# Kernel optimization log

Hardware: AMD Instinct MI355X
Metric: run time of the kernel (lower is better)

Reference implementation:

```python
import jax, jax.numpy as jnp
import numpy as np

B, H, S, D = 4, 16, 2048, 128

def setup_inputs() -> dict:
    key = jax.random.key(0)
    k1, k2, k3, k4 = jax.random.split(key, 4)
    query = jax.random.normal(k1, (B, H, S, D), dtype=jnp.float32)
    key_t = jax.random.normal(k2, (B, H, S, D), dtype=jnp.float32)
    value = jax.random.normal(k3, (B, H, S, D), dtype=jnp.float32)
    mask = jax.random.randint(k4, (B, 1, S, S), 0, 2, dtype=jnp.int32)
    return {"query": query, "key": key_t, "value": value, "mask": mask}

def reference(query, key, value, mask):
    d_k = query.shape[-1]
    scale = d_k ** 0.5
    # [B,H,S,S] attention logits
    attn_logits = jnp.einsum('bhqd,bhkd->bhqk', query, key)
    neg_inf = jnp.finfo(attn_logits.dtype).min
    attn_logits = jnp.where(mask == 0, neg_inf, attn_logits)
    attn_weights = jax.nn.softmax(attn_logits / scale, axis=-1)
    # dropout is identity in eval/inference mode
    attn_output = jnp.einsum('bhqk,bhkd->bhqd', attn_weights, value)
    return attn_output, attn_weights
```

## Files before the change

### kernel.cpp

```cpp
#include <hip/hip_runtime.h>
#include <hip/hip_bf16.h>

namespace {

constexpr int Hn = 16;
constexpr int Sn = 2048;
constexpr int Dn = 128;
constexpr int BM = 64;
constexpr int BN = 64;
constexpr int THREADS = 256;
constexpr int NT = Sn / BN;
constexpr long long OUT0 = 4LL * 16 * 2048 * 128;

constexpr int QSTR = 136;
constexpr int VSTR = 68;

typedef short s16x4 __attribute__((ext_vector_type(4)));
typedef float f32x4 __attribute__((ext_vector_type(4)));

__device__ __forceinline__ unsigned short f2bu(float x) {
    return __bfloat16_as_ushort(__float2bfloat16(x));
}
__device__ __forceinline__ unsigned pk2(float lo, float hi) {
    return (unsigned)f2bu(lo) | ((unsigned)f2bu(hi) << 16);
}

__device__ __forceinline__ void k_issue(const float* __restrict__ g, int sc, int sr,
                                        float4* v) {
#pragma unroll
    for (int it = 0; it < 4; ++it) {
        const float4* gp = reinterpret_cast<const float4*>(
            g + (size_t)(sr + 16 * it) * Dn + sc * 8);
        v[2 * it]     = gp[0];
        v[2 * it + 1] = gp[1];
    }
}
__device__ __forceinline__ void k_write(unsigned short* lds, int sc, int sr,
                                        const float4* v) {
#pragma unroll
    for (int it = 0; it < 4; ++it) {
        const int r = sr + 16 * it;
        uint4 u;
        u.x = pk2(v[2 * it].x,     v[2 * it].y);
        u.y = pk2(v[2 * it].z,     v[2 * it].w);
        u.z = pk2(v[2 * it + 1].x, v[2 * it + 1].y);
        u.w = pk2(v[2 * it + 1].z, v[2 * it + 1].w);
        *reinterpret_cast<uint4*>(reinterpret_cast<char*>(lds) + r * (QSTR * 2) + sc * 16) = u;
    }
}

__device__ __forceinline__ void v_issue(const float* __restrict__ g, int tc, int kp,
                                        float4* v) {
#pragma unroll
    for (int it = 0; it < 4; ++it) {
        const int kr = 2 * (kp + 8 * it);
        v[2 * it]     = *reinterpret_cast<const float4*>(g + (size_t)kr * Dn + 4 * tc);
        v[2 * it + 1] = *reinterpret_cast<const float4*>(g + (size_t)(kr + 1) * Dn + 4 * tc);
    }
}
__device__ __forceinline__ void v_write(unsigned short* vt, int tc, int kp,
                                        const float4* v) {
#pragma unroll
    for (int it = 0; it < 4; ++it) {
        const int kr = 2 * (kp + 8 * it);
        const float a4[4] = {v[2 * it].x, v[2 * it].y, v[2 * it].z, v[2 * it].w};
        const float b4[4] = {v[2 * it + 1].x, v[2 * it + 1].y, v[2 * it + 1].z, v[2 * it + 1].w};
#pragma unroll
        for (int j = 0; j < 4; ++j) {
            const int d = 4 * tc + j;
            *reinterpret_cast<unsigned*>(reinterpret_cast<char*>(vt) + d * (VSTR * 2) + kr * 2)
                = pk2(a4[j], b4[j]);
        }
    }
}

struct SAcc { f32x4 t[4]; };

__global__ __launch_bounds__(THREADS)
void attn_fused(const float* __restrict__ Q, const float* __restrict__ K,
                const float* __restrict__ V, const int* __restrict__ M,
                float* __restrict__ out) {
    __shared__ __align__(16) unsigned short smem[8704 * 2 + BM * VSTR];
    unsigned short* bufA = smem;
    unsigned short* bufB = smem + 8704;
    unsigned short* wlds = smem + 17408;

    const int tid  = threadIdx.x;
    const int lane = tid & 63;
    const int wv   = tid >> 6;
    const int lr   = lane & 15;
    const int lg   = lane >> 4;

    const int bh    = blockIdx.y;
    const int b     = bh >> 4;
    const int qbase = blockIdx.x * BM;

    const float* Qg = Q + ((size_t)bh * Sn + qbase) * Dn;
    const float* Kg = K + (size_t)bh * Sn * Dn;
    const float* Vg = V + (size_t)bh * Sn * Dn;
    const int*   Mg = M + ((size_t)b * Sn + qbase) * Sn;
    float*       Og = out + ((size_t)bh * Sn + qbase) * Dn;
    float*       Wg = out + OUT0 + ((size_t)bh * Sn + qbase) * Sn;

    const float scl2 = 1.4426950408889634f / 11.313708498984761f;
    const int qrow = 16 * wv + 4 * lg;

    const int sc = tid & 15, sr = tid >> 4;
    const int tc = tid & 31, kp = tid >> 5;

    const int* mrow[4];
#pragma unroll
    for (int r = 0; r < 4; ++r) mrow[r] = Mg + (size_t)(qrow + r) * Sn + lr;

    {
        float4 qv[8], kv[8];
        k_issue(Qg, sc, sr, qv);
        k_issue(Kg, sc, sr, kv);
        k_write(bufB, sc, sr, qv);
        k_write(bufA, sc, sr, kv);
    }
    __syncthreads();
    s16x4 qf[8];
#pragma unroll
    for (int dsv = 0; dsv < 8; ++dsv)
        qf[dsv] = *reinterpret_cast<const s16x4*>(
            reinterpret_cast<const char*>(bufB) + (16 * wv + lr) * (QSTR * 2) + dsv * 32 + lg * 8);
    __syncthreads();

    const f32x4 zero = {0.f, 0.f, 0.f, 0.f};

    auto qk_tile = [&](const unsigned short* kb) -> SAcc {
        SAcc s;
#pragma unroll
        for (int t = 0; t < 4; ++t) s.t[t] = zero;
#pragma unroll
        for (int dsv = 0; dsv < 8; ++dsv) {
            const int koff = dsv * 32 + lg * 8;
#pragma unroll
            for (int t = 0; t < 4; ++t) {
                const s16x4 bb = *reinterpret_cast<const s16x4*>(
                    reinterpret_cast<const char*>(kb) + (16 * t + lr) * (QSTR * 2) + koff);
                s.t[t] = __builtin_amdgcn_mfma_f32_16x16x16bf16_1k(qf[dsv], bb, s.t[t], 0, 0, 0);
            }
        }
        return s;
    };

    float rs[4] = {0.f, 0.f, 0.f, 0.f};
    for (int t = 0; t < NT; ++t) {
        unsigned short* cur = (t & 1) ? bufB : bufA;
        unsigned short* nxt = (t & 1) ? bufA : bufB;
        float4 kv[8];
        const bool pre = (t + 1 < NT);
        if (pre) k_issue(Kg + (size_t)(t + 1) * BN * Dn, sc, sr, kv);

        int mv[16];
        const int kc = t * BN;
#pragma unroll
        for (int tt = 0; tt < 4; ++tt)
#pragma unroll
            for (int r = 0; r < 4; ++r) mv[4 * tt + r] = mrow[r][kc + 16 * tt];

        SAcc s = qk_tile(cur);
#pragma unroll
        for (int tt = 0; tt < 4; ++tt)
#pragma unroll
            for (int r = 0; r < 4; ++r)
                rs[r] += mv[4 * tt + r] ? __builtin_amdgcn_exp2f(s.t[tt][r] * scl2) : 0.f;

        if (pre) k_write(nxt, sc, sr, kv);
        __syncthreads();
    }

    float inv[4];
#pragma unroll
    for (int r = 0; r < 4; ++r) {
        float v = rs[r];
        v += __shfl_xor(v, 1);
        v += __shfl_xor(v, 2);
        v += __shfl_xor(v, 4);
        v += __shfl_xor(v, 8);
        inv[r] = 1.0f / v;
    }

    {
        float4 kv0[8], vv0[8];
        k_issue(Kg, sc, sr, kv0);
        v_issue(Vg, tc, kp, vv0);
        k_write(bufA, sc, sr, kv0);
        v_write(bufB, tc, kp, vv0);
    }
    __syncthreads();

    f32x4 oacc[8];
#pragma unroll
    for (int f = 0; f < 8; ++f) oacc[f] = zero;

    for (int t = 0; t < NT; ++t) {
        float4 kv[8], vv[8];
        const bool pre = (t + 1 < NT);
        if (pre) {
            k_issue(Kg + (size_t)(t + 1) * BN * Dn, sc, sr, kv);
            v_issue(Vg + (size_t)(t + 1) * BN * Dn, tc, kp, vv);
        }

        int mv[16];
        const int kc = t * BN;
#pragma unroll
        for (int tt = 0; tt < 4; ++tt)
#pragma unroll
            for (int r = 0; r < 4; ++r) mv[4 * tt + r] = mrow[r][kc + 16 * tt];

        SAcc s = qk_tile(bufA);

#pragma unroll
        for (int tt = 0; tt < 4; ++tt) {
#pragma unroll
            for (int r = 0; r < 4; ++r) {
                const float e = mv[4 * tt + r] ? __builtin_amdgcn_exp2f(s.t[tt][r] * scl2) : 0.f;
                const float w = e * inv[r];
                Wg[(size_t)(qrow + r) * Sn + kc + 16 * tt + lr] = w;
                reinterpret_cast<unsigned short*>(
                    reinterpret_cast<char*>(wlds) + (qrow + r) * (VSTR * 2))[16 * tt + lr] = f2bu(w);
            }
        }

#pragma unroll
        for (int kk = 0; kk < 4; ++kk) {
            const int koff = kk * 32 + lg * 8;
            const s16x4 aw = *reinterpret_cast<const s16x4*>(
                reinterpret_cast<const char*>(wlds) + (16 * wv + lr) * (VSTR * 2) + koff);
#pragma unroll
            for (int f = 0; f < 8; ++f) {
                const s16x4 bv = *reinterpret_cast<const s16x4*>(
                    reinterpret_cast<const char*>(bufB) + (16 * f + lr) * (VSTR * 2) + koff);
                oacc[f] = __builtin_amdgcn_mfma_f32_16x16x16bf16_1k(aw, bv, oacc[f], 0, 0, 0);
            }
        }
        __syncthreads();
        if (pre) {
            k_write(bufA, sc, sr, kv);
            v_write(bufB, tc, kp, vv);
        }
        __syncthreads();
    }

#pragma unroll
    for (int f = 0; f < 8; ++f) {
#pragma unroll
        for (int r = 0; r < 4; ++r) {
            Og[(size_t)(qrow + r) * Dn + 16 * f + lr] = oacc[f][r];
        }
    }
}

}

extern "C" void kernel_launch(void* const* d_in, const int* in_sizes, int n_in,
                              void* d_out, int out_size, void* d_ws, size_t ws_size,
                              hipStream_t stream) {
    (void)in_sizes; (void)n_in; (void)d_ws; (void)ws_size; (void)out_size;
    const float* Q = (const float*)d_in[0];
    const float* K = (const float*)d_in[1];
    const float* V = (const float*)d_in[2];
    const int*   M = (const int*)d_in[3];
    float* out = (float*)d_out;
    dim3 grid(Sn / BM, 4 * Hn);
    attn_fused<<<grid, THREADS, 0, stream>>>(Q, K, V, M, out);
}
```

Baseline: 1.006 ms.

## Preconvert Q/K/V to swizzled bf16 and bit-pack mask before attention

Adds pre-pass kernels that convert Q (pre-scaled), K and a transposed V to bf16 in swizzled workspace layouts, and pack the int32 mask into bitmasks. The main attention kernel then streams K/V tiles straight into LDS with global_load_lds DMA double buffering, reads mask bits instead of int32 values, and normalises via a log-sum subtracted in the exponent. This removes the repeated fp32 loads, conversions and mask traffic across the two passes, at the cost of extra launches and workspace traffic. The original kernel is kept as a fallback when the workspace is too small.

```diff
diff --git a/kernel.cpp b/kernel.cpp
--- a/kernel.cpp
+++ b/kernel.cpp
@@ -3,17 +3,21 @@
 
 namespace {
 
-constexpr int Hn = 16;
 constexpr int Sn = 2048;
 constexpr int Dn = 128;
-constexpr int BM = 64;
 constexpr int BN = 64;
 constexpr int THREADS = 256;
 constexpr int NT = Sn / BN;
-constexpr long long OUT0 = 4LL * 16 * 2048 * 128;
-
-constexpr int QSTR = 136;
-constexpr int VSTR = 68;
+constexpr int NH = 64;
+constexpr long long OUT0 = 4LL * 16 * Sn * Dn;
+constexpr float QSs = 1.4426950408889634f / 11.313708498984761f;
+
+constexpr size_t HB     = (size_t)Sn * Dn * 2;
+constexpr size_t QB_OFF = 0;
+constexpr size_t KB_OFF = HB * NH;
+constexpr size_t VT_OFF = 2 * HB * NH;
+constexpr size_t MB_OFF = 3 * HB * NH;
+constexpr size_t WS_NEED = MB_OFF + (size_t)4 * Sn * 64 * 4;
 
 typedef short s16x4 __attribute__((ext_vector_type(4)));
 typedef float f32x4 __attribute__((ext_vector_type(4)));
@@ -25,8 +29,248 @@
     return (unsigned)f2bu(lo) | ((unsigned)f2bu(hi) << 16);
 }
 
-__device__ __forceinline__ void k_issue(const float* __restrict__ g, int sc, int sr,
-                                        float4* v) {
+__device__ __forceinline__ void glds16(const char* g, char* l) {
+    __builtin_amdgcn_global_load_lds(
+        (__attribute__((address_space(1))) void*)(uintptr_t)g,
+        (__attribute__((address_space(3))) void*)(uintptr_t)(unsigned)(uintptr_t)l,
+        16, 0, 0);
+}
+
+#define MFMA16(A, B, C) __builtin_amdgcn_mfma_f32_16x16x16bf16_1k((A), (B), (C), 0, 0, 0)
+
+
+__global__ __launch_bounds__(256) void cvt_rows(const float* __restrict__ src,
+                                                char* __restrict__ dst, float qs) {
+    const int x = blockIdx.x * 256 + threadIdx.x;
+    const int c = x & 15;
+    const int row = x >> 4;
+    const float4* gp = reinterpret_cast<const float4*>(src + (size_t)row * Dn + c * 8);
+    const float4 f0 = gp[0], f1 = gp[1];
+    uint4 u;
+    u.x = pk2(f0.x * qs, f0.y * qs);
+    u.y = pk2(f0.z * qs, f0.w * qs);
+    u.z = pk2(f1.x * qs, f1.y * qs);
+    u.w = pk2(f1.z * qs, f1.w * qs);
+    *reinterpret_cast<uint4*>(dst + (size_t)row * 256 + ((c * 16) ^ ((row & 7) << 4))) = u;
+}
+
+__global__ __launch_bounds__(256) void cvt_vt(const float* __restrict__ V,
+                                              char* __restrict__ vt) {
+    const int x = blockIdx.x * 256 + threadIdx.x;
+    const int d = x & 127;
+    const int kc8 = (x >> 7) & 255;
+    const int bh = x >> 15;
+    const float* s = V + (size_t)bh * Sn * Dn + (size_t)kc8 * 8 * Dn + d;
+    float f[8];
+#pragma unroll
+    for (int i = 0; i < 8; ++i) f[i] = s[(size_t)i * Dn];
+    uint4 u;
+    u.x = pk2(f[0], f[1]); u.y = pk2(f[2], f[3]);
+    u.z = pk2(f[4], f[5]); u.w = pk2(f[6], f[7]);
+    *reinterpret_cast<uint4*>(vt + (size_t)bh * HB + (size_t)(kc8 >> 3) * 16384
+                              + d * 128 + (((kc8 & 7) * 16) ^ ((d & 7) << 4))) = u;
+}
+
+__global__ __launch_bounds__(256) void mask_pack(const int* __restrict__ M,
+                                                 unsigned* __restrict__ mb) {
+    const int x = blockIdx.x * 256 + threadIdx.x;
+    const int w = x & 63;
+    const int q = (x >> 6) & 2047;
+    const int b = x >> 17;
+    const int4* p = reinterpret_cast<const int4*>(M + ((size_t)b * Sn + q) * Sn + w * 32);
+    unsigned u = 0;
+#pragma unroll
+    for (int i = 0; i < 8; ++i) {
+        const int4 v = p[i];
+        u |= (v.x != 0 ? 1u : 0u) << (4 * i);
+        u |= (v.y != 0 ? 1u : 0u) << (4 * i + 1);
+        u |= (v.z != 0 ? 1u : 0u) << (4 * i + 2);
+        u |= (v.w != 0 ? 1u : 0u) << (4 * i + 3);
+    }
+    mb[x] = u;
+}
+
+
+__global__ __launch_bounds__(THREADS, 2)
+void attn_main(const char* __restrict__ ws, const unsigned* __restrict__ mbits,
+               float* __restrict__ out) {
+    __shared__ __align__(16) char smem[74496];
+    char* kb0 = smem;
+    char* kb1 = smem + 16384;
+    char* vb0 = smem + 32768;
+    char* vb1 = smem + 49152;
+    unsigned short* wl = reinterpret_cast<unsigned short*>(smem + 65536);
+
+    const int tid  = threadIdx.x;
+    const int lane = tid & 63;
+    const int wv   = tid >> 6;
+    const int lr   = lane & 15;
+    const int lg   = lane >> 4;
+
+    const int bh    = blockIdx.y;
+    const int b     = bh >> 4;
+    const int qbase = blockIdx.x * 64;
+
+    const char* Qbh  = ws + (size_t)bh * HB;
+    const char* Kbh  = ws + KB_OFF + (size_t)bh * HB;
+    const char* Vtbh = ws + VT_OFF + (size_t)bh * HB;
+    float*      Og   = out + ((size_t)bh * Sn + qbase) * Dn;
+    float*      Wg   = out + OUT0 + ((size_t)bh * Sn + qbase) * Sn;
+
+    const int qrow = 16 * wv + 4 * lg;
+
+    const unsigned* mbase[4];
+#pragma unroll
+    for (int r = 0; r < 4; ++r)
+        mbase[r] = mbits + ((size_t)b * Sn + qbase + qrow + r) * 64;
+
+    s16x4 qf[8];
+    {
+        const char* qp = Qbh + (size_t)(qbase + 16 * wv + lr) * 256;
+#pragma unroll
+        for (int dsv = 0; dsv < 8; ++dsv)
+            qf[dsv] = *reinterpret_cast<const s16x4*>(
+                qp + ((dsv * 32 + lg * 8) ^ ((lr & 7) << 4)));
+    }
+
+    const f32x4 zero = {0.f, 0.f, 0.f, 0.f};
+
+    auto dma = [&](const char* gtile, char* buf) {
+        const char* g = gtile + wv * 4096 + lane * 16;
+        char* l = buf + wv * 4096;
+#pragma unroll
+        for (int i = 0; i < 4; ++i) glds16(g + i * 1024, l + i * 1024);
+    };
+
+    dma(Kbh, kb0);
+    __syncthreads();
+
+    float rs[4] = {0.f, 0.f, 0.f, 0.f};
+    {
+        char* kcur = kb0;
+        char* knxt = kb1;
+        for (int t = 0; t < NT; ++t) {
+            if (t + 1 < NT) dma(Kbh + (size_t)(t + 1) * 16384, knxt);
+
+            uint2 mw[4];
+#pragma unroll
+            for (int r = 0; r < 4; ++r)
+                mw[r] = *reinterpret_cast<const uint2*>(mbase[r] + 2 * t);
+
+            f32x4 s[4] = {zero, zero, zero, zero};
+#pragma unroll
+            for (int dsv = 0; dsv < 8; ++dsv) {
+                const int koff = (dsv * 32 + lg * 8) ^ ((lr & 7) << 4);
+#pragma unroll
+                for (int tt = 0; tt < 4; ++tt) {
+                    const s16x4 bb = *reinterpret_cast<const s16x4*>(
+                        kcur + (16 * tt + lr) * 256 + koff);
+                    s[tt] = MFMA16(qf[dsv], bb, s[tt]);
+                }
+            }
+#pragma unroll
+            for (int tt = 0; tt < 4; ++tt) {
+#pragma unroll
+                for (int r = 0; r < 4; ++r) {
+                    const unsigned wsel = (tt < 2) ? mw[r].x : mw[r].y;
+                    const unsigned bit = (wsel >> ((tt & 1) * 16 + lr)) & 1u;
+                    rs[r] += bit ? __builtin_amdgcn_exp2f(s[tt][r]) : 0.f;
+                }
+            }
+            __syncthreads();
+            char* tmp = kcur; kcur = knxt; knxt = tmp;
+        }
+    }
+
+    float li[4];
+#pragma unroll
+    for (int r = 0; r < 4; ++r) {
+        float v = rs[r];
+        v += __shfl_xor(v, 1);
+        v += __shfl_xor(v, 2);
+        v += __shfl_xor(v, 4);
+        v += __shfl_xor(v, 8);
+        li[r] = -__log2f(v);
+    }
+
+    dma(Kbh, kb0);
+    dma(Vtbh, vb0);
+    __syncthreads();
+
+    f32x4 oacc[8];
+#pragma unroll
+    for (int f = 0; f < 8; ++f) oacc[f] = zero;
+
+    {
+        char* kcur = kb0; char* knxt = kb1;
+        char* vcur = vb0; char* vnxt = vb1;
+        for (int t = 0; t < NT; ++t) {
+            const int kc = t * BN;
+            if (t + 1 < NT) {
+                dma(Kbh  + (size_t)(t + 1) * 16384, knxt);
+                dma(Vtbh + (size_t)(t + 1) * 16384, vnxt);
+            }
+
+            uint2 mw[4];
+#pragma unroll
+            for (int r = 0; r < 4; ++r)
+                mw[r] = *reinterpret_cast<const uint2*>(mbase[r] + 2 * t);
+
+            f32x4 s[4] = {zero, zero, zero, zero};
+#pragma unroll
+            for (int dsv = 0; dsv < 8; ++dsv) {
+                const int koff = (dsv * 32 + lg * 8) ^ ((lr & 7) << 4);
+#pragma unroll
+                for (int tt = 0; tt < 4; ++tt) {
+                    const s16x4 bb = *reinterpret_cast<const s16x4*>(
+                        kcur + (16 * tt + lr) * 256 + koff);
+                    s[tt] = MFMA16(qf[dsv], bb, s[tt]);
+                }
+            }
+
+#pragma unroll
+            for (int tt = 0; tt < 4; ++tt) {
+#pragma unroll
+                for (int r = 0; r < 4; ++r) {
+                    const unsigned wsel = (tt < 2) ? mw[r].x : mw[r].y;
+                    const unsigned bit = (wsel >> ((tt & 1) * 16 + lr)) & 1u;
+                    const float e = bit ? __builtin_amdgcn_exp2f(s[tt][r] + li[r]) : 0.f;
+                    Wg[(size_t)(qrow + r) * Sn + kc + 16 * tt + lr] = e;
+                    wl[(qrow + r) * 70 + 16 * tt + lr] = f2bu(e);
+                }
+            }
+
+#pragma unroll
+            for (int kk = 0; kk < 4; ++kk) {
+                const s16x4 aw = *reinterpret_cast<const s16x4*>(
+                    reinterpret_cast<const char*>(wl) + (16 * wv + lr) * 140 + kk * 32 + lg * 8);
+#pragma unroll
+                for (int f = 0; f < 8; ++f) {
+                    const s16x4 bv = *reinterpret_cast<const s16x4*>(
+                        vcur + (16 * f + lr) * 128 + ((kk * 32 + lg * 8) ^ ((lr & 7) << 4)));
+                    oacc[f] = MFMA16(aw, bv, oacc[f]);
+                }
+            }
+
+            __syncthreads();
+            char* tmp = kcur; kcur = knxt; knxt = tmp;
+            tmp = vcur; vcur = vnxt; vnxt = tmp;
+        }
+    }
+
+#pragma unroll
+    for (int f = 0; f < 8; ++f)
+#pragma unroll
+        for (int r = 0; r < 4; ++r)
+            Og[(size_t)(qrow + r) * Dn + 16 * f + lr] = oacc[f][r];
+}
+
+
+constexpr int FQSTR = 136;
+constexpr int FVSTR = 68;
+
+__device__ __forceinline__ void fbk_issue(const float* __restrict__ g, int sc, int sr,
+                                          float4* v) {
 #pragma unroll
     for (int it = 0; it < 4; ++it) {
         const float4* gp = reinterpret_cast<const float4*>(
@@ -35,8 +279,8 @@
         v[2 * it + 1] = gp[1];
     }
 }
-__device__ __forceinline__ void k_write(unsigned short* lds, int sc, int sr,
-                                        const float4* v) {
+__device__ __forceinline__ void fbk_write(unsigned short* lds, int sc, int sr,
+                                          const float4* v) {
 #pragma unroll
     for (int it = 0; it < 4; ++it) {
         const int r = sr + 16 * it;
@@ -45,12 +289,11 @@
         u.y = pk2(v[2 * it].z,     v[2 * it].w);
         u.z = pk2(v[2 * it + 1].x, v[2 * it + 1].y);
         u.w = pk2(v[2 * it + 1].z, v[2 * it + 1].w);
-        *reinterpret_cast<uint4*>(reinterpret_cast<char*>(lds) + r * (QSTR * 2) + sc * 16) = u;
-    }
-}
-
-__device__ __forceinline__ void v_issue(const float* __restrict__ g, int tc, int kp,
-                                        float4* v) {
+        *reinterpret_cast<uint4*>(reinterpret_cast<char*>(lds) + r * (FQSTR * 2) + sc * 16) = u;
+    }
+}
+__device__ __forceinline__ void fbv_issue(const float* __restrict__ g, int tc, int kp,
+                                          float4* v) {
 #pragma unroll
     for (int it = 0; it < 4; ++it) {
         const int kr = 2 * (kp + 8 * it);
@@ -58,8 +301,8 @@
         v[2 * it + 1] = *reinterpret_cast<const float4*>(g + (size_t)(kr + 1) * Dn + 4 * tc);
     }
 }
-__device__ __forceinline__ void v_write(unsigned short* vt, int tc, int kp,
-                                        const float4* v) {
+__device__ __forceinline__ void fbv_write(unsigned short* vt, int tc, int kp,
+                                          const float4* v) {
 #pragma unroll
     for (int it = 0; it < 4; ++it) {
         const int kr = 2 * (kp + 8 * it);
@@ -68,22 +311,20 @@
 #pragma unroll
         for (int j = 0; j < 4; ++j) {
             const int d = 4 * tc + j;
-            *reinterpret_cast<unsigned*>(reinterpret_cast<char*>(vt) + d * (VSTR * 2) + kr * 2)
+            *reinterpret_cast<unsigned*>(reinterpret_cast<char*>(vt) + d * (FVSTR * 2) + kr * 2)
                 = pk2(a4[j], b4[j]);
         }
     }
 }
 
-struct SAcc { f32x4 t[4]; };
-
-__global__ __launch_bounds__(THREADS)
-void attn_fused(const float* __restrict__ Q, const float* __restrict__ K,
-                const float* __restrict__ V, const int* __restrict__ M,
-                float* __restrict__ out) {
-    __shared__ __align__(16) unsigned short smem[8704 * 2 + BM * VSTR];
-    unsigned short* bufA = smem;
-    unsigned short* bufB = smem + 8704;
-    unsigned short* wlds = smem + 17408;
+__global__ __launch_bounds__(256)
+void attn_fb(const float* __restrict__ Q, const float* __restrict__ K,
+             const float* __restrict__ V, const int* __restrict__ M,
+             float* __restrict__ out) {
+    __shared__ __align__(16) unsigned short fsm[8704 * 2 + 64 * FVSTR];
+    unsigned short* bufA = fsm;
+    unsigned short* bufB = fsm + 8704;
+    unsigned short* wl2  = fsm + 17408;
 
     const int tid  = threadIdx.x;
     const int lane = tid & 63;
@@ -93,7 +334,7 @@
 
     const int bh    = blockIdx.y;
     const int b     = bh >> 4;
-    const int qbase = blockIdx.x * BM;
+    const int qbase = blockIdx.x * 64;
 
     const float* Qg = Q + ((size_t)bh * Sn + qbase) * Dn;
     const float* Kg = K + (size_t)bh * Sn * Dn;
@@ -102,7 +343,7 @@
     float*       Og = out + ((size_t)bh * Sn + qbase) * Dn;
     float*       Wg = out + OUT0 + ((size_t)bh * Sn + qbase) * Sn;
 
-    const float scl2 = 1.4426950408889634f / 11.313708498984761f;
+    const float scl2 = QSs;
     const int qrow = 16 * wv + 4 * lg;
 
     const int sc = tid & 15, sr = tid >> 4;
@@ -114,23 +355,23 @@
 
     {
         float4 qv[8], kv[8];
-        k_issue(Qg, sc, sr, qv);
-        k_issue(Kg, sc, sr, kv);
-        k_write(bufB, sc, sr, qv);
-        k_write(bufA, sc, sr, kv);
+        fbk_issue(Qg, sc, sr, qv);
+        fbk_issue(Kg, sc, sr, kv);
+        fbk_write(bufB, sc, sr, qv);
+        fbk_write(bufA, sc, sr, kv);
     }
     __syncthreads();
     s16x4 qf[8];
 #pragma unroll
     for (int dsv = 0; dsv < 8; ++dsv)
         qf[dsv] = *reinterpret_cast<const s16x4*>(
-            reinterpret_cast<const char*>(bufB) + (16 * wv + lr) * (QSTR * 2) + dsv * 32 + lg * 8);
+            reinterpret_cast<const char*>(bufB) + (16 * wv + lr) * (FQSTR * 2) + dsv * 32 + lg * 8);
     __syncthreads();
 
     const f32x4 zero = {0.f, 0.f, 0.f, 0.f};
 
-    auto qk_tile = [&](const unsigned short* kb) -> SAcc {
-        SAcc s;
+    auto qk_tile = [&](const unsigned short* kb) {
+        struct { f32x4 t[4]; } s;
 #pragma unroll
         for (int t = 0; t < 4; ++t) s.t[t] = zero;
 #pragma unroll
@@ -139,8 +380,8 @@
 #pragma unroll
             for (int t = 0; t < 4; ++t) {
                 const s16x4 bb = *reinterpret_cast<const s16x4*>(
-                    reinterpret_cast<const char*>(kb) + (16 * t + lr) * (QSTR * 2) + koff);
-                s.t[t] = __builtin_amdgcn_mfma_f32_16x16x16bf16_1k(qf[dsv], bb, s.t[t], 0, 0, 0);
+                    reinterpret_cast<const char*>(kb) + (16 * t + lr) * (FQSTR * 2) + koff);
+                s.t[t] = MFMA16(qf[dsv], bb, s.t[t]);
             }
         }
         return s;
@@ -152,7 +393,7 @@
         unsigned short* nxt = (t & 1) ? bufA : bufB;
         float4 kv[8];
         const bool pre = (t + 1 < NT);
-        if (pre) k_issue(Kg + (size_t)(t + 1) * BN * Dn, sc, sr, kv);
+        if (pre) fbk_issue(Kg + (size_t)(t + 1) * BN * Dn, sc, sr, kv);
 
         int mv[16];
         const int kc = t * BN;
@@ -161,14 +402,14 @@
 #pragma unroll
             for (int r = 0; r < 4; ++r) mv[4 * tt + r] = mrow[r][kc + 16 * tt];
 
-        SAcc s = qk_tile(cur);
+        auto s = qk_tile(cur);
 #pragma unroll
         for (int tt = 0; tt < 4; ++tt)
 #pragma unroll
             for (int r = 0; r < 4; ++r)
                 rs[r] += mv[4 * tt + r] ? __builtin_amdgcn_exp2f(s.t[tt][r] * scl2) : 0.f;
 
-        if (pre) k_write(nxt, sc, sr, kv);
+        if (pre) fbk_write(nxt, sc, sr, kv);
         __syncthreads();
     }
 
@@ -185,10 +426,10 @@
 
     {
         float4 kv0[8], vv0[8];
-        k_issue(Kg, sc, sr, kv0);
-        v_issue(Vg, tc, kp, vv0);
-        k_write(bufA, sc, sr, kv0);
-        v_write(bufB, tc, kp, vv0);
+        fbk_issue(Kg, sc, sr, kv0);
+        fbv_issue(Vg, tc, kp, vv0);
+        fbk_write(bufA, sc, sr, kv0);
+        fbv_write(bufB, tc, kp, vv0);
     }
     __syncthreads();
 
@@ -200,8 +441,8 @@
         float4 kv[8], vv[8];
         const bool pre = (t + 1 < NT);
         if (pre) {
-            k_issue(Kg + (size_t)(t + 1) * BN * Dn, sc, sr, kv);
-            v_issue(Vg + (size_t)(t + 1) * BN * Dn, tc, kp, vv);
+            fbk_issue(Kg + (size_t)(t + 1) * BN * Dn, sc, sr, kv);
+            fbv_issue(Vg + (size_t)(t + 1) * BN * Dn, tc, kp, vv);
         }
 
         int mv[16];
@@ -211,7 +452,7 @@
 #pragma unroll
             for (int r = 0; r < 4; ++r) mv[4 * tt + r] = mrow[r][kc + 16 * tt];
 
-        SAcc s = qk_tile(bufA);
+        auto s = qk_tile(bufA);
 
 #pragma unroll
         for (int tt = 0; tt < 4; ++tt) {
@@ -221,7 +462,7 @@
                 const float w = e * inv[r];
                 Wg[(size_t)(qrow + r) * Sn + kc + 16 * tt + lr] = w;
                 reinterpret_cast<unsigned short*>(
-                    reinterpret_cast<char*>(wlds) + (qrow + r) * (VSTR * 2))[16 * tt + lr] = f2bu(w);
+                    reinterpret_cast<char*>(wl2) + (qrow + r) * (FVSTR * 2))[16 * tt + lr] = f2bu(w);
             }
         }
 
@@ -229,29 +470,27 @@
         for (int kk = 0; kk < 4; ++kk) {
             const int koff = kk * 32 + lg * 8;
             const s16x4 aw = *reinterpret_cast<const s16x4*>(
-                reinterpret_cast<const char*>(wlds) + (16 * wv + lr) * (VSTR * 2) + koff);
+                reinterpret_cast<const char*>(wl2) + (16 * wv + lr) * (FVSTR * 2) + koff);
 #pragma unroll
             for (int f = 0; f < 8; ++f) {
                 const s16x4 bv = *reinterpret_cast<const s16x4*>(
-                    reinterpret_cast<const char*>(bufB) + (16 * f + lr) * (VSTR * 2) + koff);
-                oacc[f] = __builtin_amdgcn_mfma_f32_16x16x16bf16_1k(aw, bv, oacc[f], 0, 0, 0);
+                    reinterpret_cast<const char*>(bufB) + (16 * f + lr) * (FVSTR * 2) + koff);
+                oacc[f] = MFMA16(aw, bv, oacc[f]);
             }
         }
         __syncthreads();
         if (pre) {
-            k_write(bufA, sc, sr, kv);
-            v_write(bufB, tc, kp, vv);
+            fbk_write(bufA, sc, sr, kv);
+            fbv_write(bufB, tc, kp, vv);
         }
         __syncthreads();
     }
 
 #pragma unroll
-    for (int f = 0; f < 8; ++f) {
-#pragma unroll
-        for (int r = 0; r < 4; ++r) {
+    for (int f = 0; f < 8; ++f)
+#pragma unroll
+        for (int r = 0; r < 4; ++r)
             Og[(size_t)(qrow + r) * Dn + 16 * f + lr] = oacc[f][r];
-        }
-    }
 }
 
 }
@@ -259,12 +498,22 @@
 extern "C" void kernel_launch(void* const* d_in, const int* in_sizes, int n_in,
                               void* d_out, int out_size, void* d_ws, size_t ws_size,
                               hipStream_t stream) {
-    (void)in_sizes; (void)n_in; (void)d_ws; (void)ws_size; (void)out_size;
+    (void)in_sizes; (void)n_in; (void)out_size;
     const float* Q = (const float*)d_in[0];
     const float* K = (const float*)d_in[1];
     const float* V = (const float*)d_in[2];
     const int*   M = (const int*)d_in[3];
     float* out = (float*)d_out;
-    dim3 grid(Sn / BM, 4 * Hn);
-    attn_fused<<<grid, THREADS, 0, stream>>>(Q, K, V, M, out);
-}
+
+    if (ws_size >= WS_NEED) {
+        char* ws = (char*)d_ws;
+        cvt_rows<<<dim3(8192), dim3(256), 0, stream>>>(Q, ws + QB_OFF, QSs);
+        cvt_rows<<<dim3(8192), dim3(256), 0, stream>>>(K, ws + KB_OFF, 1.0f);
+        cvt_vt  <<<dim3(8192), dim3(256), 0, stream>>>(V, ws + VT_OFF);
+        mask_pack<<<dim3(2048), dim3(256), 0, stream>>>(M, (unsigned*)(ws + MB_OFF));
+        attn_main<<<dim3(Sn / 64, NH), dim3(THREADS), 0, stream>>>(
+            ws, (const unsigned*)(ws + MB_OFF), out);
+    } else {
+        attn_fb<<<dim3(Sn / 64, NH), dim3(256), 0, stream>>>(Q, K, V, M, out);
+    }
+}
```

Result: faster. 837.8 us, median of 2 (-16.7%).
